# Kernel tuning notes

Hardware: AMD Instinct MI355X
Metric: run time of the kernel (lower is better)

## Reference

```python
import jax, jax.numpy as jnp
import numpy as np
import math

B, S, E = 4, 2048, 1024

def setup_inputs() -> dict:
    key = jax.random.key(0)
    ks = jax.random.split(key, 12)
    scale = 1.0 / math.sqrt(E)
    inp = {
        "query": jax.random.normal(ks[0], (B, S, E), jnp.float32),
        "key_": jax.random.normal(ks[1], (B, S, E), jnp.float32),
        "value": jax.random.normal(ks[2], (B, S, E), jnp.float32),
        # causal mask, broadcast over batch: 1 = keep, 0 = mask
        "mask": jnp.broadcast_to(jnp.tril(jnp.ones((S, S), jnp.int32)), (B, S, S)),
        "Wq": jax.random.uniform(ks[3], (E, E), jnp.float32, -scale, scale),
        "bq": jax.random.uniform(ks[4], (E,), jnp.float32, -scale, scale),
        "Wk": jax.random.uniform(ks[5], (E, E), jnp.float32, -scale, scale),
        "bk": jax.random.uniform(ks[6], (E,), jnp.float32, -scale, scale),
        "Wv": jax.random.uniform(ks[7], (E, E), jnp.float32, -scale, scale),
        "bv": jax.random.uniform(ks[8], (E,), jnp.float32, -scale, scale),
        "Wo": jax.random.uniform(ks[9], (E, E), jnp.float32, -scale, scale),
        "bo": jax.random.uniform(ks[10], (E,), jnp.float32, -scale, scale),
    }
    return inp

def reference(query, key_, value, mask, Wq, bq, Wk, bk, Wv, bv, Wo, bo):
    # Linear projections (torch Linear: x @ W.T + b)
    Q = jnp.einsum('bse,fe->bsf', query, Wq) + bq
    K = jnp.einsum('bse,fe->bsf', key_, Wk) + bk
    V = jnp.einsum('bse,fe->bsf', value, Wv) + bv
    # NOTE: module never splits heads; scores over full embed_dim, scaled by sqrt(embed_dim)
    scores = jnp.einsum('bqe,bke->bqk', Q, K) / jnp.sqrt(jnp.asarray(E, Q.dtype))
    scores = jnp.where(mask == 0, -jnp.inf, scores)
    attn = jax.nn.softmax(scores, axis=-1)
    attn_out = jnp.einsum('bqk,bke->bqe', attn, V)
    return jnp.einsum('bse,fe->bsf', attn_out, Wo) + bo
```

## Files before the change

kernel.cpp:

```cpp
#include <hip/hip_runtime.h>

typedef __bf16 bf16;
typedef __attribute__((ext_vector_type(8))) __bf16 bf16x8;
typedef __attribute__((ext_vector_type(4))) __bf16 bf16x4;
typedef __attribute__((ext_vector_type(4))) float f32x4;

#define DEVINL __device__ __forceinline__

DEVINL void gload_lds16(const bf16* g, bf16* l) {
    __builtin_amdgcn_global_load_lds(
        (__attribute__((address_space(1))) unsigned int*)(unsigned long long)g,
        (__attribute__((address_space(3))) unsigned int*)l,
        16, 0, 0);
}

__global__ __launch_bounds__(256) void cvt_f32_to_bf16(
    const float* __restrict__ in, bf16* __restrict__ out, int n4) {
    int i = blockIdx.x * blockDim.x + threadIdx.x;
    if (i >= n4) return;
    float4 f = ((const float4*)in)[i];
    bf16x4 o;
    o.x = (bf16)f.x; o.y = (bf16)f.y; o.z = (bf16)f.z; o.w = (bf16)f.w;
    ((bf16x4*)out)[i] = o;
}

__global__ __launch_bounds__(256) void transpose_bf16(
    const unsigned short* __restrict__ in, unsigned short* __restrict__ out,
    int R, int C) {
    __shared__ unsigned short t[64][65];
    const size_t bo = (size_t)blockIdx.z * R * C;
    const int r0 = blockIdx.y * 64, c0 = blockIdx.x * 64;
#pragma unroll
    for (int i = 0; i < 16; i++) {
        int lin = threadIdx.x + i * 256;
        int r = lin >> 6, c = lin & 63;
        t[r][c] = in[bo + (size_t)(r0 + r) * C + (c0 + c)];
    }
    __syncthreads();
#pragma unroll
    for (int i = 0; i < 16; i++) {
        int lin = threadIdx.x + i * 256;
        int r = lin >> 6, c = lin & 63;
        out[bo + (size_t)(c0 + r) * R + (r0 + c)] = t[c][r];
    }
}

template <int EPI>
__global__ __launch_bounds__(256) void gemm_bt(
    const bf16* __restrict__ A, const bf16* __restrict__ B,
    const float* __restrict__ bias, void* __restrict__ Cv,
    int M, int N, int K,
    long long sA, long long sB, long long sC,
    float scale, int causal) {
    const int bx = blockIdx.x, by = blockIdx.y, bz = blockIdx.z;
    if (causal == 1 && bx > by) return;
    const int m0 = by * 128, n0 = bx * 128;
    int Keff = K;
    if (causal == 2) { Keff = m0 + 128; if (Keff > K) Keff = K; }

    A += (size_t)bz * sA;
    B += (size_t)bz * sB;

    __shared__ __align__(16) bf16 As[128 * 32];
    __shared__ __align__(16) bf16 Bs[128 * 32];

    const int tid = threadIdx.x;
    const int wave = tid >> 6;
    const int lane = tid & 63;
    const int lr = lane & 15;
    const int lq = lane >> 4;
    const int wm = (wave >> 1) * 64;
    const int wn = (wave & 1) * 64;

    const int srow = lane >> 2;
    const int scol = (lane & 3) * 8;

    f32x4 acc[4][4];
    const f32x4 fzero = {0.f, 0.f, 0.f, 0.f};
#pragma unroll
    for (int i = 0; i < 4; i++)
#pragma unroll
        for (int j = 0; j < 4; j++) acc[i][j] = fzero;

    for (int k0 = 0; k0 < Keff; k0 += 32) {
        const bf16* ga0 = A + (size_t)(m0 + wave * 16 + srow) * K + (k0 + scol);
        const bf16* gb0 = B + (size_t)(n0 + wave * 16 + srow) * K + (k0 + scol);
        gload_lds16(ga0,                 As + wave * 512);
        gload_lds16(ga0 + (size_t)64 * K, As + (wave + 4) * 512);
        gload_lds16(gb0,                 Bs + wave * 512);
        gload_lds16(gb0 + (size_t)64 * K, Bs + (wave + 4) * 512);
        __syncthreads();

        bf16x8 af[4], bfr[4];
#pragma unroll
        for (int i = 0; i < 4; i++)
            af[i] = *(const bf16x8*)(As + (wm + i * 16 + lr) * 32 + lq * 8);
#pragma unroll
        for (int j = 0; j < 4; j++)
            bfr[j] = *(const bf16x8*)(Bs + (wn + j * 16 + lr) * 32 + lq * 8);
#pragma unroll
        for (int i = 0; i < 4; i++)
#pragma unroll
            for (int j = 0; j < 4; j++)
                acc[i][j] = __builtin_amdgcn_mfma_f32_16x16x32_bf16(
                    af[i], bfr[j], acc[i][j], 0, 0, 0);
        __syncthreads();
    }

    if (EPI == 0) {
        bf16* C = (bf16*)Cv + (size_t)bz * sC;
#pragma unroll
        for (int j = 0; j < 4; j++) {
            const int col = n0 + wn + j * 16 + lr;
            const float bb = bias ? bias[col] : 0.0f;
#pragma unroll
            for (int i = 0; i < 4; i++) {
                const int rowb = m0 + wm + i * 16 + lq * 4;
#pragma unroll
                for (int r = 0; r < 4; r++)
                    C[(size_t)(rowb + r) * N + col] =
                        (bf16)(acc[i][j][r] * scale + bb);
            }
        }
    } else {
        float* C = (float*)Cv + (size_t)bz * sC;
#pragma unroll
        for (int j = 0; j < 4; j++) {
            const int col = n0 + wn + j * 16 + lr;
            const float bb = bias ? bias[col] : 0.0f;
#pragma unroll
            for (int i = 0; i < 4; i++) {
                const int rowb = m0 + wm + i * 16 + lq * 4;
#pragma unroll
                for (int r = 0; r < 4; r++)
                    C[(size_t)(rowb + r) * N + col] =
                        acc[i][j][r] * scale + bb;
            }
        }
    }
}

__global__ __launch_bounds__(256) void softmax_causal(
    const float* __restrict__ Sc, bf16* __restrict__ P, int S) {
    const int row = blockIdx.x;
    const int q = row & (S - 1);
    const float* src = Sc + (size_t)row * S;
    bf16* dst = P + (size_t)row * S;
    const int L = q + 1;
    const int tid = threadIdx.x;

    float v[8];
    float mx = -3.0e38f;
#pragma unroll
    for (int i = 0; i < 8; i++) {
        int k = tid + i * 256;
        v[i] = (k < L) ? src[k] : -3.0e38f;
        mx = fmaxf(mx, v[i]);
    }
#pragma unroll
    for (int off = 32; off > 0; off >>= 1) mx = fmaxf(mx, __shfl_xor(mx, off, 64));
    __shared__ float redm[4], reds[4];
    if ((tid & 63) == 0) redm[tid >> 6] = mx;
    __syncthreads();
    mx = fmaxf(fmaxf(redm[0], redm[1]), fmaxf(redm[2], redm[3]));

    float sum = 0.f;
#pragma unroll
    for (int i = 0; i < 8; i++) {
        int k = tid + i * 256;
        float e = (k < L) ? __expf(v[i] - mx) : 0.f;
        v[i] = e;
        sum += e;
    }
#pragma unroll
    for (int off = 32; off > 0; off >>= 1) sum += __shfl_xor(sum, off, 64);
    if ((tid & 63) == 0) reds[tid >> 6] = sum;
    __syncthreads();
    sum = reds[0] + reds[1] + reds[2] + reds[3];
    const float inv = 1.0f / sum;
#pragma unroll
    for (int i = 0; i < 8; i++) {
        int k = tid + i * 256;
        dst[k] = (bf16)(v[i] * inv);
    }
}

extern "C" void kernel_launch(void* const* d_in, const int* in_sizes, int n_in,
                              void* d_out, int out_size, void* d_ws, size_t ws_size,
                              hipStream_t stream) {
    const int B = 4, S = 2048, E = 1024;
    const size_t SBE = (size_t)B * S * E;
    const size_t EE = (size_t)E * E;

    const float* q_in = (const float*)d_in[0];
    const float* k_in = (const float*)d_in[1];
    const float* v_in = (const float*)d_in[2];
    const float* Wq = (const float*)d_in[4];
    const float* bq = (const float*)d_in[5];
    const float* Wk = (const float*)d_in[6];
    const float* bk = (const float*)d_in[7];
    const float* Wv = (const float*)d_in[8];
    const float* bv = (const float*)d_in[9];
    const float* Wo = (const float*)d_in[10];
    const float* bo = (const float*)d_in[11];

    char* ws = (char*)d_ws;
    bf16* qb = (bf16*)ws;
    bf16* kb = qb + SBE;
    bf16* vb = kb + SBE;
    bf16* Vb = vb + SBE;
    float* Sc = (float*)ws;
    bf16* AO = (bf16*)ws;
    char* p = ws + 4 * SBE * 2;
    bf16* Qb = (bf16*)p; p += SBE * 2;
    bf16* Kb = (bf16*)p; p += SBE * 2;
    bf16* Vt = (bf16*)p; p += SBE * 2;
    bf16* Pb = (bf16*)p; p += (size_t)B * S * S * 2;
    bf16* Wqb = (bf16*)p; p += EE * 2;
    bf16* Wkb = (bf16*)p; p += EE * 2;
    bf16* Wvb = (bf16*)p; p += EE * 2;
    bf16* Wob = (bf16*)p; p += EE * 2;

    cvt_f32_to_bf16<<<(int)(SBE / 4 / 256), 256, 0, stream>>>(q_in, qb, (int)(SBE / 4));
    cvt_f32_to_bf16<<<(int)(SBE / 4 / 256), 256, 0, stream>>>(k_in, kb, (int)(SBE / 4));
    cvt_f32_to_bf16<<<(int)(SBE / 4 / 256), 256, 0, stream>>>(v_in, vb, (int)(SBE / 4));
    cvt_f32_to_bf16<<<(int)(EE / 4 / 256), 256, 0, stream>>>(Wq, Wqb, (int)(EE / 4));
    cvt_f32_to_bf16<<<(int)(EE / 4 / 256), 256, 0, stream>>>(Wk, Wkb, (int)(EE / 4));
    cvt_f32_to_bf16<<<(int)(EE / 4 / 256), 256, 0, stream>>>(Wv, Wvb, (int)(EE / 4));
    cvt_f32_to_bf16<<<(int)(EE / 4 / 256), 256, 0, stream>>>(Wo, Wob, (int)(EE / 4));

    dim3 blk(256);
    dim3 gproj(E / 128, (B * S) / 128, 1);
    gemm_bt<0><<<gproj, blk, 0, stream>>>(qb, Wqb, bq, Qb, B * S, E, E, 0, 0, 0, 1.f, 0);
    gemm_bt<0><<<gproj, blk, 0, stream>>>(kb, Wkb, bk, Kb, B * S, E, E, 0, 0, 0, 1.f, 0);
    gemm_bt<0><<<gproj, blk, 0, stream>>>(vb, Wvb, bv, Vb, B * S, E, E, 0, 0, 0, 1.f, 0);

    dim3 gt(E / 64, S / 64, B);
    transpose_bf16<<<gt, blk, 0, stream>>>((const unsigned short*)Vb,
                                           (unsigned short*)Vt, S, E);

    dim3 gsc(S / 128, S / 128, B);
    gemm_bt<1><<<gsc, blk, 0, stream>>>(Qb, Kb, nullptr, Sc, S, S, E,
                                        (long long)S * E, (long long)S * E,
                                        (long long)S * S, 0.03125f, 1);

    softmax_causal<<<B * S, 256, 0, stream>>>(Sc, Pb, S);

    dim3 gpv(E / 128, S / 128, B);
    gemm_bt<0><<<gpv, blk, 0, stream>>>(Pb, Vt, nullptr, AO, S, E, S,
                                        (long long)S * S, (long long)E * S,
                                        (long long)S * E, 1.f, 2);

    gemm_bt<1><<<gproj, blk, 0, stream>>>(AO, Wob, bo, (float*)d_out,
                                          B * S, E, E, 0, 0, 0, 1.f, 0);
}
```

Baseline: 468.3 us.

## Shrink GEMM tiles to 128x64, batch QKV projections and conversions into single launches

```diff
diff --git a/kernel.cpp b/kernel.cpp
--- a/kernel.cpp
+++ b/kernel.cpp
@@ -14,14 +14,32 @@
         16, 0, 0);
 }
 
-__global__ __launch_bounds__(256) void cvt_f32_to_bf16(
-    const float* __restrict__ in, bf16* __restrict__ out, int n4) {
+__global__ __launch_bounds__(256) void cvt3_f32_to_bf16(
+    const float* __restrict__ a, const float* __restrict__ b,
+    const float* __restrict__ c, bf16* __restrict__ out, int n4) {
     int i = blockIdx.x * blockDim.x + threadIdx.x;
     if (i >= n4) return;
-    float4 f = ((const float4*)in)[i];
+    const float* src = (blockIdx.z == 0) ? a : (blockIdx.z == 1) ? b : c;
+    bf16* dst = out + (size_t)blockIdx.z * (size_t)n4 * 4;
+    float4 f = ((const float4*)src)[i];
     bf16x4 o;
     o.x = (bf16)f.x; o.y = (bf16)f.y; o.z = (bf16)f.z; o.w = (bf16)f.w;
-    ((bf16x4*)out)[i] = o;
+    ((bf16x4*)dst)[i] = o;
+}
+
+__global__ __launch_bounds__(256) void cvt4_f32_to_bf16(
+    const float* __restrict__ a, const float* __restrict__ b,
+    const float* __restrict__ c, const float* __restrict__ d,
+    bf16* __restrict__ out, int n4) {
+    int i = blockIdx.x * blockDim.x + threadIdx.x;
+    if (i >= n4) return;
+    const float* src = (blockIdx.z == 0) ? a : (blockIdx.z == 1) ? b
+                     : (blockIdx.z == 2) ? c : d;
+    bf16* dst = out + (size_t)blockIdx.z * (size_t)n4 * 4;
+    float4 f = ((const float4*)src)[i];
+    bf16x4 o;
+    o.x = (bf16)f.x; o.y = (bf16)f.y; o.z = (bf16)f.z; o.w = (bf16)f.w;
+    ((bf16x4*)dst)[i] = o;
 }
 
 __global__ __launch_bounds__(256) void transpose_bf16(
@@ -50,56 +68,55 @@
     const bf16* __restrict__ A, const bf16* __restrict__ B,
     const float* __restrict__ bias, void* __restrict__ Cv,
     int M, int N, int K,
-    long long sA, long long sB, long long sC,
+    long long sA, long long sB, long long sC, long long sBias,
     float scale, int causal) {
     const int bx = blockIdx.x, by = blockIdx.y, bz = blockIdx.z;
-    if (causal == 1 && bx > by) return;
-    const int m0 = by * 128, n0 = bx * 128;
+    const int m0 = by * 128, n0 = bx * 64;
+    if (causal == 1 && n0 > m0 + 127) return;
     int Keff = K;
     if (causal == 2) { Keff = m0 + 128; if (Keff > K) Keff = K; }
 
     A += (size_t)bz * sA;
     B += (size_t)bz * sB;
+    if (bias) bias += (size_t)bz * sBias;
 
     __shared__ __align__(16) bf16 As[128 * 32];
-    __shared__ __align__(16) bf16 Bs[128 * 32];
+    __shared__ __align__(16) bf16 Bs[64 * 32];
 
     const int tid = threadIdx.x;
     const int wave = tid >> 6;
     const int lane = tid & 63;
     const int lr = lane & 15;
     const int lq = lane >> 4;
-    const int wm = (wave >> 1) * 64;
-    const int wn = (wave & 1) * 64;
+    const int wm = wave * 32;
 
     const int srow = lane >> 2;
     const int scol = (lane & 3) * 8;
 
-    f32x4 acc[4][4];
+    f32x4 acc[2][4];
     const f32x4 fzero = {0.f, 0.f, 0.f, 0.f};
 #pragma unroll
-    for (int i = 0; i < 4; i++)
+    for (int i = 0; i < 2; i++)
 #pragma unroll
         for (int j = 0; j < 4; j++) acc[i][j] = fzero;
 
     for (int k0 = 0; k0 < Keff; k0 += 32) {
         const bf16* ga0 = A + (size_t)(m0 + wave * 16 + srow) * K + (k0 + scol);
         const bf16* gb0 = B + (size_t)(n0 + wave * 16 + srow) * K + (k0 + scol);
-        gload_lds16(ga0,                 As + wave * 512);
+        gload_lds16(ga0,                  As + wave * 512);
         gload_lds16(ga0 + (size_t)64 * K, As + (wave + 4) * 512);
-        gload_lds16(gb0,                 Bs + wave * 512);
-        gload_lds16(gb0 + (size_t)64 * K, Bs + (wave + 4) * 512);
+        gload_lds16(gb0,                  Bs + wave * 512);
         __syncthreads();
 
-        bf16x8 af[4], bfr[4];
-#pragma unroll
-        for (int i = 0; i < 4; i++)
+        bf16x8 af[2], bfr[4];
+#pragma unroll
+        for (int i = 0; i < 2; i++)
             af[i] = *(const bf16x8*)(As + (wm + i * 16 + lr) * 32 + lq * 8);
 #pragma unroll
         for (int j = 0; j < 4; j++)
-            bfr[j] = *(const bf16x8*)(Bs + (wn + j * 16 + lr) * 32 + lq * 8);
-#pragma unroll
-        for (int i = 0; i < 4; i++)
+            bfr[j] = *(const bf16x8*)(Bs + (j * 16 + lr) * 32 + lq * 8);
+#pragma unroll
+        for (int i = 0; i < 2; i++)
 #pragma unroll
             for (int j = 0; j < 4; j++)
                 acc[i][j] = __builtin_amdgcn_mfma_f32_16x16x32_bf16(
@@ -111,10 +128,10 @@
         bf16* C = (bf16*)Cv + (size_t)bz * sC;
 #pragma unroll
         for (int j = 0; j < 4; j++) {
-            const int col = n0 + wn + j * 16 + lr;
+            const int col = n0 + j * 16 + lr;
             const float bb = bias ? bias[col] : 0.0f;
 #pragma unroll
-            for (int i = 0; i < 4; i++) {
+            for (int i = 0; i < 2; i++) {
                 const int rowb = m0 + wm + i * 16 + lq * 4;
 #pragma unroll
                 for (int r = 0; r < 4; r++)
@@ -126,10 +143,10 @@
         float* C = (float*)Cv + (size_t)bz * sC;
 #pragma unroll
         for (int j = 0; j < 4; j++) {
-            const int col = n0 + wn + j * 16 + lr;
+            const int col = n0 + j * 16 + lr;
             const float bb = bias ? bias[col] : 0.0f;
 #pragma unroll
-            for (int i = 0; i < 4; i++) {
+            for (int i = 0; i < 2; i++) {
                 const int rowb = m0 + wm + i * 16 + lq * 4;
 #pragma unroll
                 for (int r = 0; r < 4; r++)
@@ -205,52 +222,52 @@
     const float* bo = (const float*)d_in[11];
 
     char* ws = (char*)d_ws;
-    bf16* qb = (bf16*)ws;
-    bf16* kb = qb + SBE;
-    bf16* vb = kb + SBE;
-    bf16* Vb = vb + SBE;
+    bf16* qkvb = (bf16*)ws;
     float* Sc = (float*)ws;
     bf16* AO = (bf16*)ws;
-    char* p = ws + 4 * SBE * 2;
-    bf16* Qb = (bf16*)p; p += SBE * 2;
-    bf16* Kb = (bf16*)p; p += SBE * 2;
+    char* p = ws + (size_t)B * S * S * 4;
+    bf16* QKVb = (bf16*)p; p += 3 * SBE * 2;
     bf16* Vt = (bf16*)p; p += SBE * 2;
     bf16* Pb = (bf16*)p; p += (size_t)B * S * S * 2;
-    bf16* Wqb = (bf16*)p; p += EE * 2;
-    bf16* Wkb = (bf16*)p; p += EE * 2;
-    bf16* Wvb = (bf16*)p; p += EE * 2;
-    bf16* Wob = (bf16*)p; p += EE * 2;
-
-    cvt_f32_to_bf16<<<(int)(SBE / 4 / 256), 256, 0, stream>>>(q_in, qb, (int)(SBE / 4));
-    cvt_f32_to_bf16<<<(int)(SBE / 4 / 256), 256, 0, stream>>>(k_in, kb, (int)(SBE / 4));
-    cvt_f32_to_bf16<<<(int)(SBE / 4 / 256), 256, 0, stream>>>(v_in, vb, (int)(SBE / 4));
-    cvt_f32_to_bf16<<<(int)(EE / 4 / 256), 256, 0, stream>>>(Wq, Wqb, (int)(EE / 4));
-    cvt_f32_to_bf16<<<(int)(EE / 4 / 256), 256, 0, stream>>>(Wk, Wkb, (int)(EE / 4));
-    cvt_f32_to_bf16<<<(int)(EE / 4 / 256), 256, 0, stream>>>(Wv, Wvb, (int)(EE / 4));
-    cvt_f32_to_bf16<<<(int)(EE / 4 / 256), 256, 0, stream>>>(Wo, Wob, (int)(EE / 4));
+    bf16* Wb = (bf16*)p; p += 4 * EE * 2;
+    float* biasWS = (float*)p; p += 3 * E * 4;
+
+    bf16* Qb = QKVb;
+    bf16* Vb = QKVb + 2 * SBE;
+    bf16* Wob = Wb + 3 * EE;
+
+    dim3 gcvt3((int)(SBE / 4 / 256), 1, 3);
+    cvt3_f32_to_bf16<<<gcvt3, 256, 0, stream>>>(q_in, k_in, v_in, qkvb, (int)(SBE / 4));
+    dim3 gcvt4((int)(EE / 4 / 256), 1, 4);
+    cvt4_f32_to_bf16<<<gcvt4, 256, 0, stream>>>(Wq, Wk, Wv, Wo, Wb, (int)(EE / 4));
+    hipMemcpyAsync(biasWS,         bq, E * 4, hipMemcpyDeviceToDevice, stream);
+    hipMemcpyAsync(biasWS + E,     bk, E * 4, hipMemcpyDeviceToDevice, stream);
+    hipMemcpyAsync(biasWS + 2 * E, bv, E * 4, hipMemcpyDeviceToDevice, stream);
 
     dim3 blk(256);
-    dim3 gproj(E / 128, (B * S) / 128, 1);
-    gemm_bt<0><<<gproj, blk, 0, stream>>>(qb, Wqb, bq, Qb, B * S, E, E, 0, 0, 0, 1.f, 0);
-    gemm_bt<0><<<gproj, blk, 0, stream>>>(kb, Wkb, bk, Kb, B * S, E, E, 0, 0, 0, 1.f, 0);
-    gemm_bt<0><<<gproj, blk, 0, stream>>>(vb, Wvb, bv, Vb, B * S, E, E, 0, 0, 0, 1.f, 0);
+    dim3 gproj(E / 64, (B * S) / 128, 3);
+    gemm_bt<0><<<gproj, blk, 0, stream>>>(qkvb, Wb, biasWS, QKVb,
+                                          B * S, E, E,
+                                          (long long)SBE, (long long)EE,
+                                          (long long)SBE, (long long)E, 1.f, 0);
 
     dim3 gt(E / 64, S / 64, B);
     transpose_bf16<<<gt, blk, 0, stream>>>((const unsigned short*)Vb,
                                            (unsigned short*)Vt, S, E);
 
-    dim3 gsc(S / 128, S / 128, B);
-    gemm_bt<1><<<gsc, blk, 0, stream>>>(Qb, Kb, nullptr, Sc, S, S, E,
+    dim3 gsc(S / 64, S / 128, B);
+    gemm_bt<1><<<gsc, blk, 0, stream>>>(Qb, QKVb + SBE, nullptr, Sc, S, S, E,
                                         (long long)S * E, (long long)S * E,
-                                        (long long)S * S, 0.03125f, 1);
+                                        (long long)S * S, 0, 0.03125f, 1);
 
     softmax_causal<<<B * S, 256, 0, stream>>>(Sc, Pb, S);
 
-    dim3 gpv(E / 128, S / 128, B);
+    dim3 gpv(E / 64, S / 128, B);
     gemm_bt<0><<<gpv, blk, 0, stream>>>(Pb, Vt, nullptr, AO, S, E, S,
                                         (long long)S * S, (long long)E * S,
-                                        (long long)S * E, 1.f, 2);
-
-    gemm_bt<1><<<gproj, blk, 0, stream>>>(AO, Wob, bo, (float*)d_out,
-                                          B * S, E, E, 0, 0, 0, 1.f, 0);
-}
+                                        (long long)S * E, 0, 1.f, 2);
+
+    dim3 gout(E / 64, (B * S) / 128, 1);
+    gemm_bt<1><<<gout, blk, 0, stream>>>(AO, Wob, bo, (float*)d_out,
+                                         B * S, E, E, 0, 0, 0, 0, 1.f, 0);
+}
```

After: 451.8 us. -3.5%, faster.
